# Optimization experiments

Hardware: AMD Instinct MI355X
Metric: run time of the kernel (lower is better)

Reference implementation:

```python
import jax, jax.numpy as jnp
import numpy as np

H, C = 4, 128            # GATConv heads, per-head out channels
MAX_NODES, NF = 50, 64   # generator graph size, node feature dim
N_NODES, N_EDGES, N_GRAPHS, LAT, HID = 10000, 160000, 64, 64, 128


def _p(key, i, shape):
    return jax.random.normal(jax.random.fold_in(key, i), shape, jnp.float32) * 0.05


def setup_inputs() -> dict:
    key = jax.random.key(0)
    inp = {}
    inp['x'] = jax.random.normal(jax.random.fold_in(key, 0), (N_NODES, NF), jnp.float32)
    inp['edge_index'] = jax.random.randint(jax.random.fold_in(key, 1), (2, N_EDGES), 0, N_NODES)
    inp['batch'] = jnp.sort(jax.random.randint(jax.random.fold_in(key, 2), (N_NODES,), 0, N_GRAPHS))
    inp['eps'] = jax.random.normal(jax.random.fold_in(key, 3), (N_GRAPHS, LAT), jnp.float32)
    # encoder params
    inp['We'] = _p(key, 10, (NF, HID)); inp['be'] = _p(key, 11, (HID,))
    inp['Wg'] = _p(key, 12, (3, HID, H * C))
    inp['ag_src'] = _p(key, 13, (3, H, C)); inp['ag_dst'] = _p(key, 14, (3, H, C))
    inp['bg'] = _p(key, 15, (3, C))
    inp['Wa1'] = _p(key, 16, (HID, 2 * HID)); inp['ba1'] = _p(key, 17, (2 * HID,))
    inp['Wa2'] = _p(key, 18, (2 * HID, HID)); inp['ba2'] = _p(key, 19, (HID,))
    inp['Wmu'] = _p(key, 20, (HID, LAT)); inp['bmu'] = _p(key, 21, (LAT,))
    inp['Wlv'] = _p(key, 22, (HID, LAT)); inp['blv'] = _p(key, 23, (LAT,))
    # generator params
    inp['Wn1'] = _p(key, 30, (LAT, 256)); inp['bn1'] = _p(key, 31, (256,))
    inp['Wn2'] = _p(key, 32, (256, 512)); inp['bn2'] = _p(key, 33, (512,))
    inp['Wn3'] = _p(key, 34, (512, MAX_NODES * NF)); inp['bn3'] = _p(key, 35, (MAX_NODES * NF,))
    inp['We1'] = _p(key, 36, (LAT + 2 * NF, 128)); inp['be1'] = _p(key, 37, (128,))
    inp['We2'] = _p(key, 38, (128, 64)); inp['be2'] = _p(key, 39, (64,))
    inp['We3'] = _p(key, 40, (64, 1)); inp['be3'] = _p(key, 41, (1,))
    inp['Wr1'] = _p(key, 42, (2 * NF, 64)); inp['br1'] = _p(key, 43, (64,))
    inp['Wr2'] = _p(key, 44, (64, 6)); inp['br2'] = _p(key, 45, (6,))
    return inp


def _gat(h, W, a_s, a_d, b, src, dst, N):
    # PyG GATConv: heads=4, concat=False (mean over heads), neg_slope=0.2, self-loops pre-added
    xh = (h @ W).reshape(N, H, C)                      # [N,H,C]
    es = (xh * a_s[None]).sum(-1)                      # [N,H] alpha_src component
    ed = (xh * a_d[None]).sum(-1)                      # [N,H] alpha_dst component
    e = jax.nn.leaky_relu(es[src] + ed[dst], 0.2)      # [E,H]
    m = jax.ops.segment_max(e, dst, num_segments=N)
    ex = jnp.exp(e - m[dst])
    den = jax.ops.segment_sum(ex, dst, num_segments=N)
    alpha = ex / den[dst]                              # softmax over incoming edges
    out = jax.ops.segment_sum(xh[src] * alpha[:, :, None], dst, num_segments=N)
    return out.mean(axis=1) + b                        # mean over heads + bias


def reference(x, eps, We, be, Wg, ag_src, ag_dst, bg, Wa1, ba1, Wa2, ba2,
              Wmu, bmu, Wlv, blv, Wn1, bn1, Wn2, bn2, Wn3, bn3,
              We1, be1, We2, be2, We3, be3, Wr1, br1, Wr2, br2,
              edge_index, batch):
    N = x.shape[0]
    B = eps.shape[0]
    loops = jnp.arange(N)
    src = jnp.concatenate([edge_index[0], loops])
    dst = jnp.concatenate([edge_index[1], loops])
    # PathwayEncoder
    h = jax.nn.relu(x @ We + be)
    for l in range(3):
        h = h + jax.nn.relu(_gat(h, Wg[l], ag_src[l], ag_dst[l], bg[l], src, dst, N))
    counts = jax.ops.segment_sum(jnp.ones((N,), h.dtype), batch, num_segments=B)
    sums = jax.ops.segment_sum(h, batch, num_segments=B)
    pr = sums / jnp.maximum(counts, 1.0)[:, None]      # global_mean_pool
    pr = jax.nn.relu(pr @ Wa1 + ba1) @ Wa2 + ba2       # pathway_aggregator
    # VAE head
    mu = pr @ Wmu + bmu
    logvar = pr @ Wlv + blv
    z = mu + eps * jnp.exp(0.5 * logvar)
    # PathwayGenerator (pairwise loop fully batched)
    g = jax.nn.relu(z @ Wn1 + bn1)
    g = jax.nn.relu(g @ Wn2 + bn2)
    nodes = (g @ Wn3 + bn3).reshape(B, MAX_NODES, NF)  # node_features (pre-sigmoid)
    node_probs = jax.nn.sigmoid(nodes)
    iu, ju = np.triu_indices(MAX_NODES, k=1)           # 1225 static pairs (i<j)
    ni = nodes[:, iu]                                  # [B,P,NF]
    nj = nodes[:, ju]
    P = iu.shape[0]
    zb = jnp.broadcast_to(z[:, None, :], (B, P, z.shape[-1]))
    eh = jax.nn.relu(jnp.concatenate([zb, ni, nj], -1) @ We1 + be1)
    eh = jax.nn.relu(eh @ We2 + be2)
    edge_probs = jax.nn.sigmoid(eh @ We3 + be3)[..., 0]            # [B,P]
    rh = jax.nn.relu(jnp.concatenate([ni, nj], -1) @ Wr1 + br1)
    reaction_types = jax.nn.softmax(rh @ Wr2 + br2, axis=-1)       # [B,P,6]
    return (mu, logvar, z, pr, node_probs, edge_probs, reaction_types)
```

## Files before the change

### kernel.cpp

```cpp
#include <hip/hip_runtime.h>
#include <cstddef>

#define N_NODES 10000
#define N_EDGES 160000
#define E_TOT   170000
#define N_GRAPHS 64
#define NF 64
#define HID 128
#define HC 512
#define LAT 64
#define MAXN 50
#define NPAIR 1225
#define NODESF 3200

typedef __attribute__((ext_vector_type(8))) short bf16x8;
typedef __attribute__((ext_vector_type(8))) unsigned short u16x8;
typedef __attribute__((ext_vector_type(4))) float f32x4;
typedef unsigned short u16;
typedef unsigned int u32;

__device__ __forceinline__ u16 f2b(float f) {
    u32 u = __float_as_uint(f);
    u32 r = (u + 0x7fffu + ((u >> 16) & 1u)) >> 16;
    return (u16)r;
}
__device__ __forceinline__ float b2f(u16 v) {
    return __uint_as_float(((u32)v) << 16);
}

struct PackArgs {
    const float* src[15];
    u16* dst[15];
};
#define PACK_TOTAL 344192
__global__ void pack_all_kernel(PackArgs pa) {
    int idx = blockIdx.x * 256 + threadIdx.x;
    if (idx >= PACK_TOTAL) return;
    const int base[16] = {0, 8192, 16384, 24576, 27648, 28672, 29696, 33792, 37888,
                          38912, 39936, 41984, 58368, 263168, 264192, 344192};
    const int Ns[15]   = {512, 512, 512, 128, 64, 64, 256, 128, 64, 64, 256, 512, 3200, 128, 0};
    const int dNs[15]  = {512, 512, 512, 128, 64, 64, 256, 128, 128, 128, 256, 512, 3200, 128, 0};
    const int coff[15] = {0, 0, 0, 0, 0, 0, 0, 0, 0, 64, 0, 0, 0, 0, 0};
    int s = 0;
    while (idx >= base[s + 1]) ++s;
    int i = idx - base[s];
    const float* sp = pa.src[s];
    u16* dp = pa.dst[s];
    if (s == 14) {
        u16x8 o;
#pragma unroll
        for (int j = 0; j < 8; ++j) o[j] = f2b(sp[(size_t)i * 8 + j]);
        *(u16x8*)&dp[(size_t)i * 8] = o;
        return;
    }
    int N = Ns[s];
    int g = i / N, n = i - g * N;
    u16x8 o;
#pragma unroll
    for (int j = 0; j < 8; ++j) o[j] = f2b(sp[(size_t)(g * 8 + j) * N + n]);
    *(u16x8*)&dp[((size_t)g * dNs[s] + n + coff[s]) * 8] = o;
}

__global__ void deg_kernel(const int* __restrict__ ei, int* __restrict__ deg) {
    int e = blockIdx.x * blockDim.x + threadIdx.x;
    if (e >= E_TOT) return;
    int d = (e < N_EDGES) ? ei[N_EDGES + e] : (e - N_EDGES);
    atomicAdd(&deg[d], 1);
}

__global__ void scan_kernel(const int* __restrict__ deg, int* __restrict__ rowstart) {
    __shared__ int wsum[16];
    __shared__ int carry_s;
    int lane = threadIdx.x & 63, wv = threadIdx.x >> 6;
    if (threadIdx.x == 0) carry_s = 0;
    __syncthreads();
    for (int base = 0; base < N_NODES; base += 1024) {
        int i = base + (int)threadIdx.x;
        int v = (i < N_NODES) ? deg[i] : 0;
        int s = v;
#pragma unroll
        for (int d = 1; d < 64; d <<= 1) {
            int u = __shfl_up(s, d);
            if (lane >= d) s += u;
        }
        if (lane == 63) wsum[wv] = s;
        __syncthreads();
        if (wv == 0 && lane < 16) {
            int ws = wsum[lane];
            int t2 = ws;
#pragma unroll
            for (int d = 1; d < 16; d <<= 1) {
                int u = __shfl_up(t2, d);
                if (lane >= d) t2 += u;
            }
            wsum[lane] = t2 - ws;
        }
        __syncthreads();
        int incl = s + wsum[wv] + carry_s;
        if (i < N_NODES) rowstart[i] = incl - v;
        __syncthreads();
        if (threadIdx.x == 1023) carry_s = incl;
        __syncthreads();
    }
    if (threadIdx.x == 0) rowstart[N_NODES] = carry_s;
}

__global__ void fill_kernel(const int* __restrict__ ei, const int* __restrict__ rowstart,
                            int* __restrict__ cursor, int* __restrict__ csr_src) {
    int e = blockIdx.x * blockDim.x + threadIdx.x;
    if (e >= E_TOT) return;
    int s, d;
    if (e < N_EDGES) { s = ei[e]; d = ei[N_EDGES + e]; }
    else { s = e - N_EDGES; d = s; }
    int pos = atomicAdd(&cursor[d], 1);
    csr_src[rowstart[d] + pos] = s;
}

template<int K, int NT, bool BIAS, bool RELU, bool F32OUT>
__global__ __launch_bounds__(256) void gemm_mh_kernel(const u16* __restrict__ A,
                                                      const u16* __restrict__ Wp,
                                                      const float* __restrict__ bias,
                                                      u16* __restrict__ bo,
                                                      float* __restrict__ fo) {
    __shared__ u16 AL[64 * (K + 8)];
    int t = threadIdx.x, w = t >> 6, l = t & 63, lr = l & 15, lg = l >> 4;
    int rb = blockIdx.x * 64, j0 = blockIdx.y * 128;
    for (int u = t; u < 64 * (K / 8); u += 256) {
        int r = u / (K / 8), c8 = (u % (K / 8)) * 8;
        int row = min(rb + r, N_NODES - 1);
        *(u16x8*)&AL[r * (K + 8) + c8] = *(const u16x8*)&A[(size_t)row * K + c8];
    }
    __syncthreads();
    f32x4 acc[4][2];
#pragma unroll
    for (int rt = 0; rt < 4; ++rt)
#pragma unroll
        for (int ct = 0; ct < 2; ++ct) acc[rt][ct] = (f32x4){0.f, 0.f, 0.f, 0.f};
#pragma unroll
    for (int ks = 0; ks < K / 32; ++ks) {
        bf16x8 a[4], b[2];
#pragma unroll
        for (int rt = 0; rt < 4; ++rt)
            a[rt] = *(const bf16x8*)&AL[(rt * 16 + lr) * (K + 8) + ks * 32 + lg * 8];
#pragma unroll
        for (int ct = 0; ct < 2; ++ct) {
            int col = j0 + w * 32 + ct * 16 + lr;
            b[ct] = *(const bf16x8*)&Wp[(size_t)((ks * 4 + lg) * NT + col) * 8];
        }
#pragma unroll
        for (int rt = 0; rt < 4; ++rt)
#pragma unroll
            for (int ct = 0; ct < 2; ++ct)
                acc[rt][ct] = __builtin_amdgcn_mfma_f32_16x16x32_bf16(a[rt], b[ct], acc[rt][ct], 0, 0, 0);
    }
#pragma unroll
    for (int rt = 0; rt < 4; ++rt)
#pragma unroll
        for (int ct = 0; ct < 2; ++ct) {
            int col = j0 + w * 32 + ct * 16 + lr;
            float bj = BIAS ? bias[col] : 0.f;
#pragma unroll
            for (int i = 0; i < 4; ++i) {
                int row = rb + rt * 16 + lg * 4 + i;
                if (row < N_NODES) {
                    float v = acc[rt][ct][i] + bj;
                    if (RELU) v = fmaxf(v, 0.f);
                    bo[(size_t)row * NT + col] = f2b(v);
                    if (F32OUT) fo[(size_t)row * NT + col] = v;
                }
            }
        }
}

template<int K, int G, int ACT, bool SPLIT>
__global__ __launch_bounds__(256) void gemm64_kernel(const u16* __restrict__ A,
                                                     const u16* __restrict__ Wp,
                                                     const float* __restrict__ bias,
                                                     const float* __restrict__ bias2,
                                                     float* __restrict__ fo,
                                                     float* __restrict__ fo2,
                                                     u16* __restrict__ bo, int N) {
    constexpr int CG = 4 / G, NB = CG * 16, Kc = K / G, KS = Kc / 32;
    constexpr int ABYTES = 64 * (K + 8) * 2;
    constexpr int LDSB = (ABYTES > 16384) ? ABYTES : 16384;
    __shared__ float LDSf[LDSB / 4];
    u16* AL = (u16*)LDSf;
    float* RB = LDSf;
    int t = threadIdx.x, w = t >> 6, l = t & 63, lr = l & 15, lg = l >> 4;
    for (int u = t; u < 64 * (K / 8); u += 256) {
        int r = u / (K / 8), c8 = (u % (K / 8)) * 8;
        *(u16x8*)&AL[r * (K + 8) + c8] = *(const u16x8*)&A[(size_t)r * K + c8];
    }
    __syncthreads();
    int kg = w % G, cg = w / G;
    int col = blockIdx.x * NB + cg * 16 + lr;
    f32x4 acc[4];
#pragma unroll
    for (int rt = 0; rt < 4; ++rt) acc[rt] = (f32x4){0.f, 0.f, 0.f, 0.f};
#pragma unroll
    for (int ks = 0; ks < KS; ++ks) {
        int k0 = kg * Kc + ks * 32;
        bf16x8 b = *(const bf16x8*)&Wp[(size_t)(((k0 >> 3) + lg) * N + col) * 8];
#pragma unroll
        for (int rt = 0; rt < 4; ++rt) {
            bf16x8 a = *(const bf16x8*)&AL[(rt * 16 + lr) * (K + 8) + k0 + lg * 8];
            acc[rt] = __builtin_amdgcn_mfma_f32_16x16x32_bf16(a, b, acc[rt], 0, 0, 0);
        }
    }
    __syncthreads();
#pragma unroll
    for (int rt = 0; rt < 4; ++rt)
#pragma unroll
        for (int i = 0; i < 4; ++i)
            RB[w * 1024 + (rt * 16 + lg * 4 + i) * 16 + lr] = acc[rt][i];
    __syncthreads();
    for (int e = t; e < 64 * NB; e += 256) {
        int row = e / NB, cb = e - row * NB;
        int cg2 = cb >> 4, cl = cb & 15;
        float s = 0.f;
#pragma unroll
        for (int kg2 = 0; kg2 < G; ++kg2)
            s += RB[(cg2 * G + kg2) * 1024 + row * 16 + cl];
        int c = blockIdx.x * NB + cb;
        float bj;
        if (SPLIT) bj = (c < 64) ? bias[c] : bias2[c - 64];
        else bj = bias[c];
        float v = s + bj;
        if (ACT == 1) v = fmaxf(v, 0.f);
        if (bo) bo[(size_t)row * N + c] = f2b(v);
        if (SPLIT) {
            if (c < 64) fo[row * 64 + c] = v;
            else fo2[row * 64 + (c - 64)] = v;
        } else if (fo) {
            float ov = (ACT == 2) ? 1.f / (1.f + __expf(-v)) : v;
            fo[(size_t)row * N + c] = ov;
        }
    }
}

template<int K, int N, typename EP>
__device__ __forceinline__ void mm64(const u16* __restrict__ AL, int lda,
                                     const u16* __restrict__ Wp, EP ep) {
    int t = threadIdx.x, w = t >> 6, l = t & 63, lr = l & 15, lg = l >> 4;
#pragma unroll
    for (int p = 0; p < N / 64; ++p) {
        int col = p * 64 + w * 16 + lr;
        f32x4 acc[4];
#pragma unroll
        for (int rt = 0; rt < 4; ++rt) acc[rt] = (f32x4){0.f, 0.f, 0.f, 0.f};
#pragma unroll
        for (int ks = 0; ks < K / 32; ++ks) {
            bf16x8 b = *(const bf16x8*)&Wp[(size_t)((ks * 4 + lg) * N + col) * 8];
#pragma unroll
            for (int rt = 0; rt < 4; ++rt) {
                bf16x8 a = *(const bf16x8*)&AL[(rt * 16 + lr) * lda + ks * 32 + lg * 8];
                acc[rt] = __builtin_amdgcn_mfma_f32_16x16x32_bf16(a, b, acc[rt], 0, 0, 0);
            }
        }
#pragma unroll
        for (int rt = 0; rt < 4; ++rt)
#pragma unroll
            for (int i = 0; i < 4; ++i)
                ep(rt * 16 + lg * 4 + i, col, acc[rt][i]);
    }
}

__global__ __launch_bounds__(256) void fused_vae_kernel(
    const u16* __restrict__ pr0b, const float* __restrict__ eps,
    const u16* __restrict__ Wa1p, const float* __restrict__ ba1,
    const u16* __restrict__ Wa2p, const float* __restrict__ ba2,
    const u16* __restrict__ Wmulvp, const float* __restrict__ bmu, const float* __restrict__ blv,
    const u16* __restrict__ Wn1p, const float* __restrict__ bn1,
    const u16* __restrict__ Wn2p, const float* __restrict__ bn2,
    float* __restrict__ pr_o, float* __restrict__ mu_o, float* __restrict__ lv_o,
    float* __restrict__ z_o, u16* __restrict__ zbf, u16* __restrict__ g2bb) {
    __shared__ u16 P[64 * 136];
    __shared__ u16 T[64 * 272];
    __shared__ u16 Z[64 * 72];
    float* MVf = (float*)T;
    int t = threadIdx.x;
    for (int idx = t; idx < 8192; idx += 256) {
        int g = idx >> 7, c = idx & 127;
        P[g * 136 + c] = pr0b[idx];
    }
    __syncthreads();
    mm64<128, 256>(P, 136, Wa1p, [&](int row, int col, float v) {
        T[row * 272 + col] = f2b(fmaxf(v + ba1[col], 0.f));
    });
    __syncthreads();
    mm64<256, 128>(T, 272, Wa2p, [&](int row, int col, float v) {
        v += ba2[col];
        pr_o[row * 128 + col] = v;
        P[row * 136 + col] = f2b(v);
    });
    __syncthreads();
    mm64<128, 128>(P, 136, Wmulvp, [&](int row, int col, float v) {
        v += (col < 64) ? bmu[col] : blv[col - 64];
        MVf[row * 136 + col] = v;
        if (col < 64) mu_o[row * 64 + col] = v;
        else lv_o[row * 64 + (col - 64)] = v;
    });
    __syncthreads();
    for (int idx = t; idx < 4096; idx += 256) {
        int g = idx >> 6, c = idx & 63;
        float m = MVf[g * 136 + c], lvv = MVf[g * 136 + 64 + c];
        float zv = fmaf(eps[idx], __expf(0.5f * lvv), m);
        z_o[idx] = zv;
        u16 zb16 = f2b(zv);
        zbf[idx] = zb16;
        Z[g * 72 + c] = zb16;
    }
    __syncthreads();
    mm64<64, 256>(Z, 72, Wn1p, [&](int row, int col, float v) {
        T[row * 272 + col] = f2b(fmaxf(v + bn1[col], 0.f));
    });
    __syncthreads();
    mm64<256, 512>(T, 272, Wn2p, [&](int row, int col, float v) {
        g2bb[row * 512 + col] = f2b(fmaxf(v + bn2[col], 0.f));
    });
}

__global__ void esed_kernel(const u16* __restrict__ xhb, const float* __restrict__ ags,
                            const float* __restrict__ agd, float* __restrict__ es,
                            float* __restrict__ ed) {
    int wv = threadIdx.x >> 6, lane = threadIdx.x & 63;
    int n = blockIdx.x * 4 + wv;
    if (n >= N_NODES) return;
    u16x8 v = *(const u16x8*)&xhb[(size_t)n * 512 + lane * 8];
    float ps = 0.f, pd = 0.f;
#pragma unroll
    for (int j = 0; j < 8; ++j) {
        float f = b2f(v[j]);
        ps = fmaf(f, ags[lane * 8 + j], ps);
        pd = fmaf(f, agd[lane * 8 + j], pd);
    }
#pragma unroll
    for (int off = 1; off < 16; off <<= 1) {
        ps += __shfl_xor(ps, off);
        pd += __shfl_xor(pd, off);
    }
    if ((lane & 15) == 0) {
        es[n * 4 + (lane >> 4)] = ps;
        ed[n * 4 + (lane >> 4)] = pd;
    }
}

__global__ __launch_bounds__(64) void gat_agg_kernel(const u16* __restrict__ xhb,
                               const float* __restrict__ es, const float* __restrict__ ed,
                               const int* __restrict__ rowstart, const int* __restrict__ csr_src,
                               const float* __restrict__ bg, float* __restrict__ h,
                               u16* __restrict__ hb) {
    __shared__ float aL[64][4];
    __shared__ int sL[64];
    int n = blockIdx.x;
    int lane = threadIdx.x;
    int r0 = rowstart[n], r1 = rowstart[n + 1];
    int deg = r1 - r0;
    const float4 ed4 = ((const float4*)ed)[n];
    const float edh[4] = {ed4.x, ed4.y, ed4.z, ed4.w};
    float mx[4] = {-3.4e38f, -3.4e38f, -3.4e38f, -3.4e38f};
    for (int j = lane; j < deg; j += 64) {
        int s = csr_src[r0 + j];
        const float4 e4 = ((const float4*)es)[s];
        const float ev[4] = {e4.x, e4.y, e4.z, e4.w};
#pragma unroll
        for (int hh = 0; hh < 4; ++hh) {
            float e = ev[hh] + edh[hh];
            e = e > 0.f ? e : 0.2f * e;
            mx[hh] = fmaxf(mx[hh], e);
        }
    }
#pragma unroll
    for (int hh = 0; hh < 4; ++hh)
        for (int off = 32; off; off >>= 1) mx[hh] = fmaxf(mx[hh], __shfl_xor(mx[hh], off));
    float den[4] = {0.f, 0.f, 0.f, 0.f};
    for (int j = lane; j < deg; j += 64) {
        int s = csr_src[r0 + j];
        const float4 e4 = ((const float4*)es)[s];
        const float ev[4] = {e4.x, e4.y, e4.z, e4.w};
#pragma unroll
        for (int hh = 0; hh < 4; ++hh) {
            float e = ev[hh] + edh[hh];
            e = e > 0.f ? e : 0.2f * e;
            den[hh] += __expf(e - mx[hh]);
        }
    }
#pragma unroll
    for (int hh = 0; hh < 4; ++hh) {
        for (int off = 32; off; off >>= 1) den[hh] += __shfl_xor(den[hh], off);
        den[hh] = 1.f / den[hh];
    }
    float acc[8] = {0.f, 0.f, 0.f, 0.f, 0.f, 0.f, 0.f, 0.f};
    int head = lane >> 4, c0 = (lane & 15) * 8;
    for (int base = 0; base < deg; base += 64) {
        int j = base + lane;
        if (j < deg) {
            int s = csr_src[r0 + j];
            sL[lane] = s;
            const float4 e4 = ((const float4*)es)[s];
            const float ev[4] = {e4.x, e4.y, e4.z, e4.w};
            float al[4];
#pragma unroll
            for (int hh = 0; hh < 4; ++hh) {
                float e = ev[hh] + edh[hh];
                e = e > 0.f ? e : 0.2f * e;
                al[hh] = __expf(e - mx[hh]) * den[hh];
            }
            *(float4*)&aL[lane][0] = make_float4(al[0], al[1], al[2], al[3]);
        }
        __syncthreads();
        int cnt = min(64, deg - base);
        for (int j2 = 0; j2 < cnt; ++j2) {
            int s = sL[j2];
            float al = aL[j2][head];
            u16x8 v = *(const u16x8*)&xhb[(size_t)s * 512 + head * 128 + c0];
#pragma unroll
            for (int m = 0; m < 8; ++m) acc[m] = fmaf(al, b2f(v[m]), acc[m]);
        }
        __syncthreads();
    }
#pragma unroll
    for (int m = 0; m < 8; ++m) {
        float v = acc[m];
        v += __shfl_xor(v, 16);
        v += __shfl_xor(v, 32);
        acc[m] = v;
    }
    if (lane < 16) {
        float o8[8];
        u16x8 b8;
#pragma unroll
        for (int m = 0; m < 8; ++m) {
            int c = lane * 8 + m;
            float o = acc[m] * 0.25f + bg[c];
            o = fmaxf(o, 0.f);
            float hn = h[(size_t)n * 128 + c] + o;
            o8[m] = hn;
            b8[m] = f2b(hn);
        }
        *(float4*)&h[(size_t)n * 128 + lane * 8] = make_float4(o8[0], o8[1], o8[2], o8[3]);
        *(float4*)&h[(size_t)n * 128 + lane * 8 + 4] = make_float4(o8[4], o8[5], o8[6], o8[7]);
        *(u16x8*)&hb[(size_t)n * 128 + lane * 8] = b8;
    }
}

__global__ __launch_bounds__(1024) void pool_kernel2(const float* __restrict__ h,
                                                     const int* __restrict__ batch,
                                                     u16* __restrict__ pr0b) {
    __shared__ float red[8][128];
    int g = blockIdx.x;
    int t = threadIdx.x;
    int c = t & 127, rg = t >> 7;
    int lo = 0, hi = N_NODES;
    while (lo < hi) { int m = (lo + hi) >> 1; if (batch[m] < g) lo = m + 1; else hi = m; }
    int s = lo;
    lo = 0; hi = N_NODES;
    while (lo < hi) { int m = (lo + hi) >> 1; if (batch[m] < g + 1) lo = m + 1; else hi = m; }
    int e = lo;
    float acc = 0.f;
    for (int n = s + rg; n < e; n += 8) acc += h[(size_t)n * HID + c];
    red[rg][c] = acc;
    __syncthreads();
    if (rg == 0) {
        float sum = ((red[0][c] + red[1][c]) + (red[2][c] + red[3][c])) +
                    ((red[4][c] + red[5][c]) + (red[6][c] + red[7][c]));
        float cn = fmaxf((float)(e - s), 1.f);
        pr0b[g * HID + c] = f2b(sum / cn);
    }
}

__global__ void pairs_kernel(int* __restrict__ pi, int* __restrict__ pj) {
    int p = blockIdx.x * blockDim.x + threadIdx.x;
    if (p >= NPAIR) return;
    int i = 0, off = 0;
    while (off + (MAXN - 1 - i) <= p) { off += MAXN - 1 - i; ++i; }
    pi[p] = i;
    pj[p] = i + 1 + (p - off);
}

__global__ __launch_bounds__(256) void edge_react_mfma(
    const u16* __restrict__ zb, const u16* __restrict__ nb,
    const int* __restrict__ pi, const int* __restrict__ pj,
    const u16* __restrict__ We1p, const float* __restrict__ be1,
    const u16* __restrict__ We2p, const float* __restrict__ be2,
    const float* __restrict__ We3, const float* __restrict__ be3,
    const u16* __restrict__ Wr1p, const float* __restrict__ br1,
    const float* __restrict__ Wr2, const float* __restrict__ br2,
    float* __restrict__ edgep, float* __restrict__ react) {
    __shared__ u16 inA[64 * 200];
    __shared__ u16 h1A[64 * 136];
    __shared__ u16 rhA[64 * 68];
    int t = threadIdx.x, w = t >> 6, l = t & 63, lr = l & 15, lg = l >> 4;
    int b = blockIdx.y, p0 = blockIdx.x * 64;
    for (int u = t; u < 1536; u += 256) {
        int r = u / 24, c8 = (u % 24) * 8;
        int p = min(p0 + r, NPAIR - 1);
        const u16* src;
        if (c8 < 64) src = zb + b * 64 + c8;
        else if (c8 < 128) src = nb + b * NODESF + pi[p] * 64 + (c8 - 64);
        else src = nb + b * NODESF + pj[p] * 64 + (c8 - 128);
        *(u16x8*)&inA[r * 200 + c8] = *(const u16x8*)src;
    }
    __syncthreads();
    f32x4 a1[4][2];
#pragma unroll
    for (int rt = 0; rt < 4; ++rt)
#pragma unroll
        for (int ct = 0; ct < 2; ++ct) a1[rt][ct] = (f32x4){0.f, 0.f, 0.f, 0.f};
#pragma unroll
    for (int ks = 0; ks < 6; ++ks) {
        bf16x8 af[4], bf_[2];
#pragma unroll
        for (int rt = 0; rt < 4; ++rt)
            af[rt] = *(const bf16x8*)&inA[(rt * 16 + lr) * 200 + ks * 32 + lg * 8];
#pragma unroll
        for (int ct = 0; ct < 2; ++ct) {
            int col = w * 32 + ct * 16 + lr;
            bf_[ct] = *(const bf16x8*)&We1p[(size_t)((ks * 4 + lg) * 128 + col) * 8];
        }
#pragma unroll
        for (int rt = 0; rt < 4; ++rt)
#pragma unroll
            for (int ct = 0; ct < 2; ++ct)
                a1[rt][ct] = __builtin_amdgcn_mfma_f32_16x16x32_bf16(af[rt], bf_[ct], a1[rt][ct], 0, 0, 0);
    }
    f32x4 r1[4];
#pragma unroll
    for (int rt = 0; rt < 4; ++rt) r1[rt] = (f32x4){0.f, 0.f, 0.f, 0.f};
#pragma unroll
    for (int ks = 0; ks < 4; ++ks) {
        bf16x8 af[4];
#pragma unroll
        for (int rt = 0; rt < 4; ++rt)
            af[rt] = *(const bf16x8*)&inA[(rt * 16 + lr) * 200 + 64 + ks * 32 + lg * 8];
        int col = w * 16 + lr;
        bf16x8 bf_ = *(const bf16x8*)&Wr1p[(size_t)((ks * 4 + lg) * 64 + col) * 8];
#pragma unroll
        for (int rt = 0; rt < 4; ++rt)
            r1[rt] = __builtin_amdgcn_mfma_f32_16x16x32_bf16(af[rt], bf_, r1[rt], 0, 0, 0);
    }
#pragma unroll
    for (int rt = 0; rt < 4; ++rt)
#pragma unroll
        for (int ct = 0; ct < 2; ++ct) {
            int col = w * 32 + ct * 16 + lr;
            float bia = be1[col];
#pragma unroll
            for (int i = 0; i < 4; ++i) {
                int row = rt * 16 + lg * 4 + i;
                h1A[row * 136 + col] = f2b(fmaxf(a1[rt][ct][i] + bia, 0.f));
            }
        }
#pragma unroll
    for (int rt = 0; rt < 4; ++rt) {
        int col = w * 16 + lr;
        float bia = br1[col];
#pragma unroll
        for (int i = 0; i < 4; ++i) {
            int row = rt * 16 + lg * 4 + i;
            rhA[row * 68 + col] = f2b(fmaxf(r1[rt][i] + bia, 0.f));
        }
    }
    __syncthreads();
    f32x4 a2[4];
#pragma unroll
    for (int rt = 0; rt < 4; ++rt) a2[rt] = (f32x4){0.f, 0.f, 0.f, 0.f};
#pragma unroll
    for (int ks = 0; ks < 4; ++ks) {
        bf16x8 af[4];
#pragma unroll
        for (int rt = 0; rt < 4; ++rt)
            af[rt] = *(const bf16x8*)&h1A[(rt * 16 + lr) * 136 + ks * 32 + lg * 8];
        int col = w * 16 + lr;
        bf16x8 bf_ = *(const bf16x8*)&We2p[(size_t)((ks * 4 + lg) * 64 + col) * 8];
#pragma unroll
        for (int rt = 0; rt < 4; ++rt)
            a2[rt] = __builtin_amdgcn_mfma_f32_16x16x32_bf16(af[rt], bf_, a2[rt], 0, 0, 0);
    }
    u16* h2A = inA;
#pragma unroll
    for (int rt = 0; rt < 4; ++rt) {
        int col = w * 16 + lr;
        float bia = be2[col];
#pragma unroll
        for (int i = 0; i < 4; ++i) {
            int row = rt * 16 + lg * 4 + i;
            h2A[row * 68 + col] = f2b(fmaxf(a2[rt][i] + bia, 0.f));
        }
    }
    __syncthreads();
    int r = t >> 2, sub = t & 3;
    int p = p0 + r;
    float acc3 = 0.f;
#pragma unroll
    for (int kk = 0; kk < 16; ++kk) {
        int c = sub * 16 + kk;
        acc3 = fmaf(b2f(h2A[r * 68 + c]), We3[c], acc3);
    }
    acc3 += __shfl_xor(acc3, 1);
    acc3 += __shfl_xor(acc3, 2);
    if (sub == 0 && p < NPAIR)
        edgep[b * NPAIR + p] = 1.f / (1.f + __expf(-(acc3 + be3[0])));
    float lg6[6] = {0.f, 0.f, 0.f, 0.f, 0.f, 0.f};
#pragma unroll
    for (int kk = 0; kk < 16; ++kk) {
        int c = sub * 16 + kk;
        float v = b2f(rhA[r * 68 + c]);
#pragma unroll
        for (int m = 0; m < 6; ++m) lg6[m] = fmaf(v, Wr2[c * 6 + m], lg6[m]);
    }
#pragma unroll
    for (int m = 0; m < 6; ++m) {
        lg6[m] += __shfl_xor(lg6[m], 1);
        lg6[m] += __shfl_xor(lg6[m], 2);
    }
    if (sub == 0 && p < NPAIR) {
        float mx = -3.4e38f;
#pragma unroll
        for (int m = 0; m < 6; ++m) { lg6[m] += br2[m]; mx = fmaxf(mx, lg6[m]); }
        float s = 0.f;
        float ex[6];
#pragma unroll
        for (int m = 0; m < 6; ++m) { ex[m] = __expf(lg6[m] - mx); s += ex[m]; }
        float rs = 1.f / s;
#pragma unroll
        for (int m = 0; m < 6; ++m) react[(size_t)(b * NPAIR + p) * 6 + m] = ex[m] * rs;
    }
}

extern "C" void kernel_launch(void* const* d_in, const int* in_sizes, int n_in,
                              void* d_out, int out_size, void* d_ws, size_t ws_size,
                              hipStream_t stream) {
    const float* x     = (const float*)d_in[0];
    const int*   ei    = (const int*)d_in[1];
    const int*   batch = (const int*)d_in[2];
    const float* eps   = (const float*)d_in[3];
    const float* We    = (const float*)d_in[4];
    const float* be    = (const float*)d_in[5];
    const float* Wg    = (const float*)d_in[6];
    const float* ags   = (const float*)d_in[7];
    const float* agd   = (const float*)d_in[8];
    const float* bg    = (const float*)d_in[9];
    const float* Wa1   = (const float*)d_in[10];
    const float* ba1   = (const float*)d_in[11];
    const float* Wa2   = (const float*)d_in[12];
    const float* ba2   = (const float*)d_in[13];
    const float* Wmu   = (const float*)d_in[14];
    const float* bmu   = (const float*)d_in[15];
    const float* Wlv   = (const float*)d_in[16];
    const float* blv   = (const float*)d_in[17];
    const float* Wn1   = (const float*)d_in[18];
    const float* bn1   = (const float*)d_in[19];
    const float* Wn2   = (const float*)d_in[20];
    const float* bn2   = (const float*)d_in[21];
    const float* Wn3   = (const float*)d_in[22];
    const float* bn3   = (const float*)d_in[23];
    const float* We1   = (const float*)d_in[24];
    const float* be1   = (const float*)d_in[25];
    const float* We2   = (const float*)d_in[26];
    const float* be2   = (const float*)d_in[27];
    const float* We3   = (const float*)d_in[28];
    const float* be3   = (const float*)d_in[29];
    const float* Wr1   = (const float*)d_in[30];
    const float* br1   = (const float*)d_in[31];
    const float* Wr2   = (const float*)d_in[32];
    const float* br2   = (const float*)d_in[33];

    float* out = (float*)d_out;
    float* mu_o    = out;
    float* lv_o    = out + 4096;
    float* z_o     = out + 8192;
    float* pr_o    = out + 12288;
    float* nodep_o = out + 20480;
    float* edgep_o = out + 225280;
    float* react_o = out + 303680;

    float* F = (float*)d_ws;
    size_t o = 0;
    float* h  = F + o; o += (size_t)N_NODES * HID;
    float* es = F + o; o += (size_t)N_NODES * 4;
    float* ed = F + o; o += (size_t)N_NODES * 4;
    u16* U = (u16*)(F + o);
    size_t uo = 0;
    u16* hb     = U + uo; uo += (size_t)N_NODES * HID;
    u16* xb     = U + uo; uo += (size_t)N_NODES * NF;
    u16* xhb    = U + uo; uo += (size_t)N_NODES * HC;
    u16* zbf    = U + uo; uo += 4096;
    u16* nbf    = U + uo; uo += 64 * NODESF;
    u16* pr0b   = U + uo; uo += 64 * HID;
    u16* g2bb   = U + uo; uo += 64 * 512;
    u16* Wgp    = U + uo; uo += (size_t)3 * 16 * 512 * 8;
    u16* We1p   = U + uo; uo += 24 * 128 * 8;
    u16* We2p   = U + uo; uo += 16 * 64 * 8;
    u16* Wr1p   = U + uo; uo += 16 * 64 * 8;
    u16* Wa1p   = U + uo; uo += 16 * 256 * 8;
    u16* Wa2p   = U + uo; uo += 32 * 128 * 8;
    u16* Wmulvp = U + uo; uo += 16 * 128 * 8;
    u16* Wn1p   = U + uo; uo += 8 * 256 * 8;
    u16* Wn2p   = U + uo; uo += 32 * 512 * 8;
    u16* Wn3p   = U + uo; uo += (size_t)64 * 3200 * 8;
    u16* Wep    = U + uo; uo += 8 * 128 * 8;
    if (uo & 7) uo += 8 - (uo & 7);
    int* I = (int*)(U + uo);
    int* rowstart = I;
    int* csr_src  = I + (N_NODES + 1);
    int* piA      = I + (N_NODES + 1) + E_TOT;
    int* pjA      = piA + NPAIR;
    int* deg      = pjA + NPAIR;
    int* cursor   = deg + N_NODES;

    hipMemsetAsync(deg, 0, (size_t)N_NODES * 2 * sizeof(int), stream);

    PackArgs pa;
    pa.src[0] = Wg;               pa.dst[0] = Wgp;
    pa.src[1] = Wg + 65536;       pa.dst[1] = Wgp + 65536;
    pa.src[2] = Wg + 131072;      pa.dst[2] = Wgp + 131072;
    pa.src[3] = We1;              pa.dst[3] = We1p;
    pa.src[4] = We2;              pa.dst[4] = We2p;
    pa.src[5] = Wr1;              pa.dst[5] = Wr1p;
    pa.src[6] = Wa1;              pa.dst[6] = Wa1p;
    pa.src[7] = Wa2;              pa.dst[7] = Wa2p;
    pa.src[8] = Wmu;              pa.dst[8] = Wmulvp;
    pa.src[9] = Wlv;              pa.dst[9] = Wmulvp;
    pa.src[10] = Wn1;             pa.dst[10] = Wn1p;
    pa.src[11] = Wn2;             pa.dst[11] = Wn2p;
    pa.src[12] = Wn3;             pa.dst[12] = Wn3p;
    pa.src[13] = We;              pa.dst[13] = Wep;
    pa.src[14] = x;               pa.dst[14] = xb;
    pack_all_kernel<<<(PACK_TOTAL + 255) / 256, 256, 0, stream>>>(pa);

    pairs_kernel<<<5, 256, 0, stream>>>(piA, pjA);
    deg_kernel<<<(E_TOT + 255) / 256, 256, 0, stream>>>(ei, deg);
    scan_kernel<<<1, 1024, 0, stream>>>(deg, rowstart);
    fill_kernel<<<(E_TOT + 255) / 256, 256, 0, stream>>>(ei, rowstart, cursor, csr_src);

    gemm_mh_kernel<64, 128, true, true, true>
        <<<dim3((N_NODES + 63) / 64, 1), 256, 0, stream>>>(xb, Wep, be, hb, h);

    for (int l = 0; l < 3; ++l) {
        gemm_mh_kernel<128, 512, false, false, false>
            <<<dim3((N_NODES + 63) / 64, 4), 256, 0, stream>>>(
                hb, Wgp + (size_t)l * 65536, nullptr, xhb, nullptr);
        esed_kernel<<<N_NODES / 4, 256, 0, stream>>>(xhb, ags + l * HC, agd + l * HC, es, ed);
        gat_agg_kernel<<<N_NODES, 64, 0, stream>>>(xhb, es, ed, rowstart, csr_src,
                                                   bg + l * HID, h, hb);
    }

    pool_kernel2<<<N_GRAPHS, 1024, 0, stream>>>(h, batch, pr0b);

    fused_vae_kernel<<<1, 256, 0, stream>>>(
        pr0b, eps, Wa1p, ba1, Wa2p, ba2, Wmulvp, bmu, blv,
        Wn1p, bn1, Wn2p, bn2, pr_o, mu_o, lv_o, z_o, zbf, g2bb);

    gemm64_kernel<512, 4, 2, false><<<200, 256, 0, stream>>>(
        g2bb, Wn3p, bn3, nullptr, nodep_o, nullptr, nbf, 3200);

    edge_react_mfma<<<dim3(20, 64), 256, 0, stream>>>(
        zbf, nbf, piA, pjA, We1p, be1, We2p, be2, We3, be3,
        Wr1p, br1, Wr2, br2, edgep_o, react_o);
}
```

Measured before the change: 259.0 us.

## Fuse attention-score dots into GAT GEMM epilogue and merge setup kernels

Computes the per-head source and destination attention scores inside the GAT projection GEMM epilogue, using shuffle reductions and a small LDS buffer, so the separate esed kernel no longer re-reads the projected features. Folds the pair-index and degree-count kernels into the weight-packing launch to save launches. Rewrites the aggregation kernel to handle four nodes per 256-thread block, with wave shuffles replacing LDS and barriers for broadcasting neighbour indices and coefficients. The scores now come from fp32 accumulators instead of bf16-rounded values, so results may shift slightly. The epilogue also gains register pressure and a block-wide barrier.

```diff
diff --git a/kernel.cpp b/kernel.cpp
--- a/kernel.cpp
+++ b/kernel.cpp
@@ -33,9 +33,25 @@
     u16* dst[15];
 };
 #define PACK_TOTAL 344192
-__global__ void pack_all_kernel(PackArgs pa) {
+#define PACK_GRID_TOTAL (PACK_TOTAL + NPAIR + E_TOT)
+__global__ void pack_all_kernel(PackArgs pa, int* __restrict__ pi, int* __restrict__ pj,
+                                const int* __restrict__ ei, int* __restrict__ deg) {
     int idx = blockIdx.x * 256 + threadIdx.x;
-    if (idx >= PACK_TOTAL) return;
+    if (idx >= PACK_GRID_TOTAL) return;
+    if (idx >= PACK_TOTAL) {
+        int r = idx - PACK_TOTAL;
+        if (r < NPAIR) {
+            int i = 0, off = 0;
+            while (off + (MAXN - 1 - i) <= r) { off += MAXN - 1 - i; ++i; }
+            pi[r] = i;
+            pj[r] = i + 1 + (r - off);
+        } else {
+            int e = r - NPAIR;
+            int d = (e < N_EDGES) ? ei[N_EDGES + e] : (e - N_EDGES);
+            atomicAdd(&deg[d], 1);
+        }
+        return;
+    }
     const int base[16] = {0, 8192, 16384, 24576, 27648, 28672, 29696, 33792, 37888,
                           38912, 39936, 41984, 58368, 263168, 264192, 344192};
     const int Ns[15]   = {512, 512, 512, 128, 64, 64, 256, 128, 64, 64, 256, 512, 3200, 128, 0};
@@ -61,13 +77,6 @@
     *(u16x8*)&dp[((size_t)g * dNs[s] + n + coff[s]) * 8] = o;
 }
 
-__global__ void deg_kernel(const int* __restrict__ ei, int* __restrict__ deg) {
-    int e = blockIdx.x * blockDim.x + threadIdx.x;
-    if (e >= E_TOT) return;
-    int d = (e < N_EDGES) ? ei[N_EDGES + e] : (e - N_EDGES);
-    atomicAdd(&deg[d], 1);
-}
-
 __global__ void scan_kernel(const int* __restrict__ deg, int* __restrict__ rowstart) {
     __shared__ int wsum[16];
     __shared__ int carry_s;
@@ -116,13 +125,19 @@
     csr_src[rowstart[d] + pos] = s;
 }
 
-template<int K, int NT, bool BIAS, bool RELU, bool F32OUT>
+template<int K, int NT, bool BIAS, bool RELU, bool F32OUT, bool ESED>
 __global__ __launch_bounds__(256) void gemm_mh_kernel(const u16* __restrict__ A,
                                                       const u16* __restrict__ Wp,
                                                       const float* __restrict__ bias,
                                                       u16* __restrict__ bo,
-                                                      float* __restrict__ fo) {
+                                                      float* __restrict__ fo,
+                                                      const float* __restrict__ agsl,
+                                                      const float* __restrict__ agdl,
+                                                      float* __restrict__ es,
+                                                      float* __restrict__ ed) {
     __shared__ u16 AL[64 * (K + 8)];
+    __shared__ float esP[4][64];
+    __shared__ float edP[4][64];
     int t = threadIdx.x, w = t >> 6, l = t & 63, lr = l & 15, lg = l >> 4;
     int rb = blockIdx.x * 64, j0 = blockIdx.y * 128;
     for (int u = t; u < 64 * (K / 8); u += 256) {
@@ -153,12 +168,19 @@
             for (int ct = 0; ct < 2; ++ct)
                 acc[rt][ct] = __builtin_amdgcn_mfma_f32_16x16x32_bf16(a[rt], b[ct], acc[rt][ct], 0, 0, 0);
     }
+    float esp[16], edp[16];
+    if (ESED) {
+#pragma unroll
+        for (int q = 0; q < 16; ++q) { esp[q] = 0.f; edp[q] = 0.f; }
+    }
 #pragma unroll
     for (int rt = 0; rt < 4; ++rt)
 #pragma unroll
         for (int ct = 0; ct < 2; ++ct) {
             int col = j0 + w * 32 + ct * 16 + lr;
             float bj = BIAS ? bias[col] : 0.f;
+            float av = ESED ? agsl[col] : 0.f;
+            float dv = ESED ? agdl[col] : 0.f;
 #pragma unroll
             for (int i = 0; i < 4; ++i) {
                 int row = rb + rt * 16 + lg * 4 + i;
@@ -167,9 +189,41 @@
                     if (RELU) v = fmaxf(v, 0.f);
                     bo[(size_t)row * NT + col] = f2b(v);
                     if (F32OUT) fo[(size_t)row * NT + col] = v;
+                    if (ESED) {
+                        esp[rt * 4 + i] = fmaf(v, av, esp[rt * 4 + i]);
+                        edp[rt * 4 + i] = fmaf(v, dv, edp[rt * 4 + i]);
+                    }
                 }
             }
         }
+    if (ESED) {
+#pragma unroll
+        for (int q = 0; q < 16; ++q) {
+#pragma unroll
+            for (int off = 1; off < 16; off <<= 1) {
+                esp[q] += __shfl_xor(esp[q], off);
+                edp[q] += __shfl_xor(edp[q], off);
+            }
+        }
+        if (lr == 0) {
+#pragma unroll
+            for (int rt = 0; rt < 4; ++rt)
+#pragma unroll
+                for (int i = 0; i < 4; ++i) {
+                    int row = rt * 16 + lg * 4 + i;
+                    esP[w][row] = esp[rt * 4 + i];
+                    edP[w][row] = edp[rt * 4 + i];
+                }
+        }
+        __syncthreads();
+        if (t < 64) {
+            int row = rb + t;
+            if (row < N_NODES) {
+                es[row * 4 + blockIdx.y] = (esP[0][t] + esP[1][t]) + (esP[2][t] + esP[3][t]);
+                ed[row * 4 + blockIdx.y] = (edP[0][t] + edP[1][t]) + (edP[2][t] + edP[3][t]);
+            }
+        }
+    }
 }
 
 template<int K, int G, int ACT, bool SPLIT>
@@ -320,40 +374,14 @@
     });
 }
 
-__global__ void esed_kernel(const u16* __restrict__ xhb, const float* __restrict__ ags,
-                            const float* __restrict__ agd, float* __restrict__ es,
-                            float* __restrict__ ed) {
-    int wv = threadIdx.x >> 6, lane = threadIdx.x & 63;
-    int n = blockIdx.x * 4 + wv;
-    if (n >= N_NODES) return;
-    u16x8 v = *(const u16x8*)&xhb[(size_t)n * 512 + lane * 8];
-    float ps = 0.f, pd = 0.f;
-#pragma unroll
-    for (int j = 0; j < 8; ++j) {
-        float f = b2f(v[j]);
-        ps = fmaf(f, ags[lane * 8 + j], ps);
-        pd = fmaf(f, agd[lane * 8 + j], pd);
-    }
-#pragma unroll
-    for (int off = 1; off < 16; off <<= 1) {
-        ps += __shfl_xor(ps, off);
-        pd += __shfl_xor(pd, off);
-    }
-    if ((lane & 15) == 0) {
-        es[n * 4 + (lane >> 4)] = ps;
-        ed[n * 4 + (lane >> 4)] = pd;
-    }
-}
-
-__global__ __launch_bounds__(64) void gat_agg_kernel(const u16* __restrict__ xhb,
+__global__ __launch_bounds__(256) void gat_agg_kernel(const u16* __restrict__ xhb,
                                const float* __restrict__ es, const float* __restrict__ ed,
                                const int* __restrict__ rowstart, const int* __restrict__ csr_src,
                                const float* __restrict__ bg, float* __restrict__ h,
                                u16* __restrict__ hb) {
-    __shared__ float aL[64][4];
-    __shared__ int sL[64];
-    int n = blockIdx.x;
-    int lane = threadIdx.x;
+    int wv = threadIdx.x >> 6, lane = threadIdx.x & 63;
+    int n = blockIdx.x * 4 + wv;
+    if (n >= N_NODES) return;
     int r0 = rowstart[n], r1 = rowstart[n + 1];
     int deg = r1 - r0;
     const float4 ed4 = ((const float4*)ed)[n];
@@ -394,10 +422,11 @@
     int head = lane >> 4, c0 = (lane & 15) * 8;
     for (int base = 0; base < deg; base += 64) {
         int j = base + lane;
+        int sj = 0;
+        float a0 = 0.f, a1 = 0.f, a2 = 0.f, a3 = 0.f;
         if (j < deg) {
-            int s = csr_src[r0 + j];
-            sL[lane] = s;
-            const float4 e4 = ((const float4*)es)[s];
+            sj = csr_src[r0 + j];
+            const float4 e4 = ((const float4*)es)[sj];
             const float ev[4] = {e4.x, e4.y, e4.z, e4.w};
             float al[4];
 #pragma unroll
@@ -406,18 +435,18 @@
                 e = e > 0.f ? e : 0.2f * e;
                 al[hh] = __expf(e - mx[hh]) * den[hh];
             }
-            *(float4*)&aL[lane][0] = make_float4(al[0], al[1], al[2], al[3]);
-        }
-        __syncthreads();
+            a0 = al[0]; a1 = al[1]; a2 = al[2]; a3 = al[3];
+        }
         int cnt = min(64, deg - base);
         for (int j2 = 0; j2 < cnt; ++j2) {
-            int s = sL[j2];
-            float al = aL[j2][head];
+            int s = __shfl(sj, j2);
+            float b0 = __shfl(a0, j2), b1 = __shfl(a1, j2);
+            float b2 = __shfl(a2, j2), b3 = __shfl(a3, j2);
+            float al = (head < 2) ? ((head == 0) ? b0 : b1) : ((head == 2) ? b2 : b3);
             u16x8 v = *(const u16x8*)&xhb[(size_t)s * 512 + head * 128 + c0];
 #pragma unroll
             for (int m = 0; m < 8; ++m) acc[m] = fmaf(al, b2f(v[m]), acc[m]);
         }
-        __syncthreads();
     }
 #pragma unroll
     for (int m = 0; m < 8; ++m) {
@@ -467,15 +496,6 @@
         float cn = fmaxf((float)(e - s), 1.f);
         pr0b[g * HID + c] = f2b(sum / cn);
     }
-}
-
-__global__ void pairs_kernel(int* __restrict__ pi, int* __restrict__ pj) {
-    int p = blockIdx.x * blockDim.x + threadIdx.x;
-    if (p >= NPAIR) return;
-    int i = 0, off = 0;
-    while (off + (MAXN - 1 - i) <= p) { off += MAXN - 1 - i; ++i; }
-    pi[p] = i;
-    pj[p] = i + 1 + (p - off);
 }
 
 __global__ __launch_bounds__(256) void edge_react_mfma(
@@ -727,23 +747,22 @@
     pa.src[12] = Wn3;             pa.dst[12] = Wn3p;
     pa.src[13] = We;              pa.dst[13] = Wep;
     pa.src[14] = x;               pa.dst[14] = xb;
-    pack_all_kernel<<<(PACK_TOTAL + 255) / 256, 256, 0, stream>>>(pa);
-
-    pairs_kernel<<<5, 256, 0, stream>>>(piA, pjA);
-    deg_kernel<<<(E_TOT + 255) / 256, 256, 0, stream>>>(ei, deg);
+    pack_all_kernel<<<(PACK_GRID_TOTAL + 255) / 256, 256, 0, stream>>>(pa, piA, pjA, ei, deg);
+
     scan_kernel<<<1, 1024, 0, stream>>>(deg, rowstart);
     fill_kernel<<<(E_TOT + 255) / 256, 256, 0, stream>>>(ei, rowstart, cursor, csr_src);
 
-    gemm_mh_kernel<64, 128, true, true, true>
-        <<<dim3((N_NODES + 63) / 64, 1), 256, 0, stream>>>(xb, Wep, be, hb, h);
+    gemm_mh_kernel<64, 128, true, true, true, false>
+        <<<dim3((N_NODES + 63) / 64, 1), 256, 0, stream>>>(
+            xb, Wep, be, hb, h, nullptr, nullptr, nullptr, nullptr);
 
     for (int l = 0; l < 3; ++l) {
-        gemm_mh_kernel<128, 512, false, false, false>
+        gemm_mh_kernel<128, 512, false, false, false, true>
             <<<dim3((N_NODES + 63) / 64, 4), 256, 0, stream>>>(
-                hb, Wgp + (size_t)l * 65536, nullptr, xhb, nullptr);
-        esed_kernel<<<N_NODES / 4, 256, 0, stream>>>(xhb, ags + l * HC, agd + l * HC, es, ed);
-        gat_agg_kernel<<<N_NODES, 64, 0, stream>>>(xhb, es, ed, rowstart, csr_src,
-                                                   bg + l * HID, h, hb);
+                hb, Wgp + (size_t)l * 65536, nullptr, xhb, nullptr,
+                ags + l * HC, agd + l * HC, es, ed);
+        gat_agg_kernel<<<(N_NODES + 3) / 4, 256, 0, stream>>>(
+            xhb, es, ed, rowstart, csr_src, bg + l * HID, h, hb);
     }
 
     pool_kernel2<<<N_GRAPHS, 1024, 0, stream>>>(h, batch, pr0b);
```

New measurement: 278.1 us. +7.3%, slower.

## Fuse setup kernels into pack and use single-pass unnormalized softmax in GAT aggregation

Applied to the files above, without the earlier changes.

Folds the pair-index and degree-count kernels into the weight packing kernel, removing two launches. In the GAT aggregation, drops the separate max and denominator passes over each node's neighbours. It accumulates unnormalized exp weights, reduces the denominator per chunk with shuffles, and normalizes once at the end. Skipping the max subtraction relies on clamping logits at 80, which risks overflow or precision loss for larger logits.

```diff
diff --git a/kernel.cpp b/kernel.cpp
--- a/kernel.cpp
+++ b/kernel.cpp
@@ -33,9 +33,25 @@
     u16* dst[15];
 };
 #define PACK_TOTAL 344192
-__global__ void pack_all_kernel(PackArgs pa) {
+#define PACK_GRID_TOTAL (PACK_TOTAL + NPAIR + E_TOT)
+__global__ void pack_all_kernel(PackArgs pa, int* __restrict__ pi, int* __restrict__ pj,
+                                const int* __restrict__ ei, int* __restrict__ deg) {
     int idx = blockIdx.x * 256 + threadIdx.x;
-    if (idx >= PACK_TOTAL) return;
+    if (idx >= PACK_GRID_TOTAL) return;
+    if (idx >= PACK_TOTAL) {
+        int r = idx - PACK_TOTAL;
+        if (r < NPAIR) {
+            int i = 0, off = 0;
+            while (off + (MAXN - 1 - i) <= r) { off += MAXN - 1 - i; ++i; }
+            pi[r] = i;
+            pj[r] = i + 1 + (r - off);
+        } else {
+            int e = r - NPAIR;
+            int d = (e < N_EDGES) ? ei[N_EDGES + e] : (e - N_EDGES);
+            atomicAdd(&deg[d], 1);
+        }
+        return;
+    }
     const int base[16] = {0, 8192, 16384, 24576, 27648, 28672, 29696, 33792, 37888,
                           38912, 39936, 41984, 58368, 263168, 264192, 344192};
     const int Ns[15]   = {512, 512, 512, 128, 64, 64, 256, 128, 64, 64, 256, 512, 3200, 128, 0};
@@ -59,13 +75,6 @@
 #pragma unroll
     for (int j = 0; j < 8; ++j) o[j] = f2b(sp[(size_t)(g * 8 + j) * N + n]);
     *(u16x8*)&dp[((size_t)g * dNs[s] + n + coff[s]) * 8] = o;
-}
-
-__global__ void deg_kernel(const int* __restrict__ ei, int* __restrict__ deg) {
-    int e = blockIdx.x * blockDim.x + threadIdx.x;
-    if (e >= E_TOT) return;
-    int d = (e < N_EDGES) ? ei[N_EDGES + e] : (e - N_EDGES);
-    atomicAdd(&deg[d], 1);
 }
 
 __global__ void scan_kernel(const int* __restrict__ deg, int* __restrict__ rowstart) {
@@ -358,56 +367,36 @@
     int deg = r1 - r0;
     const float4 ed4 = ((const float4*)ed)[n];
     const float edh[4] = {ed4.x, ed4.y, ed4.z, ed4.w};
-    float mx[4] = {-3.4e38f, -3.4e38f, -3.4e38f, -3.4e38f};
-    for (int j = lane; j < deg; j += 64) {
-        int s = csr_src[r0 + j];
-        const float4 e4 = ((const float4*)es)[s];
-        const float ev[4] = {e4.x, e4.y, e4.z, e4.w};
-#pragma unroll
-        for (int hh = 0; hh < 4; ++hh) {
-            float e = ev[hh] + edh[hh];
-            e = e > 0.f ? e : 0.2f * e;
-            mx[hh] = fmaxf(mx[hh], e);
-        }
-    }
-#pragma unroll
-    for (int hh = 0; hh < 4; ++hh)
-        for (int off = 32; off; off >>= 1) mx[hh] = fmaxf(mx[hh], __shfl_xor(mx[hh], off));
     float den[4] = {0.f, 0.f, 0.f, 0.f};
-    for (int j = lane; j < deg; j += 64) {
-        int s = csr_src[r0 + j];
-        const float4 e4 = ((const float4*)es)[s];
-        const float ev[4] = {e4.x, e4.y, e4.z, e4.w};
-#pragma unroll
-        for (int hh = 0; hh < 4; ++hh) {
-            float e = ev[hh] + edh[hh];
-            e = e > 0.f ? e : 0.2f * e;
-            den[hh] += __expf(e - mx[hh]);
-        }
-    }
-#pragma unroll
-    for (int hh = 0; hh < 4; ++hh) {
-        for (int off = 32; off; off >>= 1) den[hh] += __shfl_xor(den[hh], off);
-        den[hh] = 1.f / den[hh];
-    }
     float acc[8] = {0.f, 0.f, 0.f, 0.f, 0.f, 0.f, 0.f, 0.f};
     int head = lane >> 4, c0 = (lane & 15) * 8;
     for (int base = 0; base < deg; base += 64) {
         int j = base + lane;
+        float ex0 = 0.f, ex1 = 0.f, ex2 = 0.f, ex3 = 0.f;
         if (j < deg) {
-            int s = csr_src[r0 + j];
-            sL[lane] = s;
-            const float4 e4 = ((const float4*)es)[s];
+            int sj = csr_src[r0 + j];
+            sL[lane] = sj;
+            const float4 e4 = ((const float4*)es)[sj];
             const float ev[4] = {e4.x, e4.y, e4.z, e4.w};
-            float al[4];
+            float exv[4];
 #pragma unroll
             for (int hh = 0; hh < 4; ++hh) {
                 float e = ev[hh] + edh[hh];
                 e = e > 0.f ? e : 0.2f * e;
-                al[hh] = __expf(e - mx[hh]) * den[hh];
+                e = fminf(e, 80.f);
+                exv[hh] = __expf(e);
             }
-            *(float4*)&aL[lane][0] = make_float4(al[0], al[1], al[2], al[3]);
-        }
+            *(float4*)&aL[lane][0] = make_float4(exv[0], exv[1], exv[2], exv[3]);
+            ex0 = exv[0]; ex1 = exv[1]; ex2 = exv[2]; ex3 = exv[3];
+        }
+#pragma unroll
+        for (int off = 32; off; off >>= 1) {
+            ex0 += __shfl_xor(ex0, off);
+            ex1 += __shfl_xor(ex1, off);
+            ex2 += __shfl_xor(ex2, off);
+            ex3 += __shfl_xor(ex3, off);
+        }
+        den[0] += ex0; den[1] += ex1; den[2] += ex2; den[3] += ex3;
         __syncthreads();
         int cnt = min(64, deg - base);
         for (int j2 = 0; j2 < cnt; ++j2) {
@@ -419,9 +408,10 @@
         }
         __syncthreads();
     }
+    float rden = 1.f / den[head];
 #pragma unroll
     for (int m = 0; m < 8; ++m) {
-        float v = acc[m];
+        float v = acc[m] * rden;
         v += __shfl_xor(v, 16);
         v += __shfl_xor(v, 32);
         acc[m] = v;
@@ -467,15 +457,6 @@
         float cn = fmaxf((float)(e - s), 1.f);
         pr0b[g * HID + c] = f2b(sum / cn);
     }
-}
-
-__global__ void pairs_kernel(int* __restrict__ pi, int* __restrict__ pj) {
-    int p = blockIdx.x * blockDim.x + threadIdx.x;
-    if (p >= NPAIR) return;
-    int i = 0, off = 0;
-    while (off + (MAXN - 1 - i) <= p) { off += MAXN - 1 - i; ++i; }
-    pi[p] = i;
-    pj[p] = i + 1 + (p - off);
 }
 
 __global__ __launch_bounds__(256) void edge_react_mfma(
@@ -727,10 +708,8 @@
     pa.src[12] = Wn3;             pa.dst[12] = Wn3p;
     pa.src[13] = We;              pa.dst[13] = Wep;
     pa.src[14] = x;               pa.dst[14] = xb;
-    pack_all_kernel<<<(PACK_TOTAL + 255) / 256, 256, 0, stream>>>(pa);
-
-    pairs_kernel<<<5, 256, 0, stream>>>(piA, pjA);
-    deg_kernel<<<(E_TOT + 255) / 256, 256, 0, stream>>>(ei, deg);
+    pack_all_kernel<<<(PACK_GRID_TOTAL + 255) / 256, 256, 0, stream>>>(pa, piA, pjA, ei, deg);
+
     scan_kernel<<<1, 1024, 0, stream>>>(deg, rowstart);
     fill_kernel<<<(E_TOT + 255) / 256, 256, 0, stream>>>(ei, rowstart, cursor, csr_src);
 
```

New measurement: 247.4 us. 1.05x faster.
